# Performance work log

Hardware: AMD Instinct MI355X
Metric: run time of the kernel (lower is better)

Reference implementation:

```python
import jax, jax.numpy as jnp
import numpy as np

# dims: L layers, T steps, N envs, D d_model, H heads, DH d_head, M mem_len, DI d_inner
L, T, N, D, H, DH, M, DI = 6, 128, 32, 1024, 16, 64, 128, 4096


def _layer_norm(x, g, b, eps=1e-5):
    mu = jnp.mean(x, axis=-1, keepdims=True)
    var = jnp.mean(jnp.square(x - mu), axis=-1, keepdims=True)
    return (x - mu) * jax.lax.rsqrt(var + eps) * g + b


def _rel_shift(x):
    # x: (n, h, q, k) with k axis indexed by relative distance (k-1 .. 0)
    n, h, q, k = x.shape
    x = jnp.pad(x, ((0, 0), (0, 0), (0, 0), (1, 0)))
    x = x.reshape(n, h, k + 1, q)[:, :, 1:, :].reshape(n, h, q, k)
    return x


def setup_inputs() -> dict:
    key = jax.random.key(0)
    ks = jax.random.split(key, 16)
    s = 0.02
    inp = {
        "x": jax.random.normal(ks[0], (T * N, D), jnp.float32),
        "context": jax.random.normal(ks[1], (T * N, D), jnp.float32),
        "mems": jax.random.normal(ks[2], (L, N, M, D), jnp.float32),
        "masks": jnp.ones((T * N,), jnp.float32),
        "Wq": jax.random.normal(ks[3], (L, D, H * DH), jnp.float32) * s,
        "Wk": jax.random.normal(ks[4], (L, D, H * DH), jnp.float32) * s,
        "Wv": jax.random.normal(ks[5], (L, D, H * DH), jnp.float32) * s,
        "Wr": jax.random.normal(ks[6], (L, D, H * DH), jnp.float32) * s,
        "Wo": jax.random.normal(ks[7], (L, H * DH, D), jnp.float32) * s,
        "W1": jax.random.normal(ks[8], (L, D, DI), jnp.float32) * s,
        "b1": jnp.zeros((L, DI), jnp.float32),
        "W2": jax.random.normal(ks[9], (L, DI, D), jnp.float32) * s,
        "b2": jnp.zeros((L, D), jnp.float32),
        "ln1_g": jnp.ones((L, D), jnp.float32),
        "ln1_b": jnp.zeros((L, D), jnp.float32),
        "ln2_g": jnp.ones((L, D), jnp.float32),
        "ln2_b": jnp.zeros((L, D), jnp.float32),
        "r_w_bias": jax.random.normal(ks[10], (H, DH), jnp.float32) * s,
        "r_r_bias": jax.random.normal(ks[11], (H, DH), jnp.float32) * s,
    }
    return inp


def reference(x, context, mems, masks, Wq, Wk, Wv, Wr, Wo, W1, b1, W2, b2,
              ln1_g, ln1_b, ln2_g, ln2_b, r_w_bias, r_r_bias):
    n = mems.shape[1]
    t = x.shape[0] // n
    m = mems.shape[2]
    klen = m + t
    dh = r_w_bias.shape[-1]
    h_heads = r_w_bias.shape[0]

    xs = x.reshape(t, n, -1)
    ctx = context.reshape(t, n, -1)
    mk = masks.reshape(t, n)

    # zero memories for envs that reset at the first step (mems * masks)
    mems = mems * mk[0][None, :, None, None]

    # episode-reset attention mask: token i attends token j iff j<=i and no
    # reset (mask==0) happened between them; memory visible only before any reset
    ep = jnp.cumsum((mk == 0.0).astype(jnp.int32), axis=0)  # (t, n)
    epT = ep.T  # (n, t)
    causal = jnp.tril(jnp.ones((t, t), bool))
    allow_seq = causal[None, :, :] & (epT[:, :, None] == epT[:, None, :])  # (n,t,t)
    allow_mem = jnp.broadcast_to((epT == 0)[:, :, None], (n, t, m))  # (n,t,m)
    allow = jnp.concatenate([allow_mem, allow_seq], axis=-1)[:, None]  # (n,1,t,K)

    # sinusoidal relative position embedding, distances klen-1 .. 0
    pos = jnp.arange(klen - 1, -1, -1, dtype=x.dtype)
    inv_freq = 1.0 / (10000.0 ** (jnp.arange(0, xs.shape[-1], 2, dtype=x.dtype) / xs.shape[-1]))
    ang = pos[:, None] * inv_freq[None, :]
    R = jnp.concatenate([jnp.sin(ang), jnp.cos(ang)], axis=-1)  # (K, D)

    h = xs + ctx  # fuse observation features with goal context
    scale = 1.0 / jnp.sqrt(jnp.asarray(dh, x.dtype))

    n_layer = mems.shape[0]
    for l in range(n_layer):
        cat = jnp.concatenate([jnp.transpose(mems[l], (1, 0, 2)), h], axis=0)  # (K,n,D)
        q = (h @ Wq[l]).reshape(t, n, h_heads, dh)
        k = (cat @ Wk[l]).reshape(klen, n, h_heads, dh)
        v = (cat @ Wv[l]).reshape(klen, n, h_heads, dh)
        r = (R @ Wr[l]).reshape(klen, h_heads, dh)
        AC = jnp.einsum('inhd,jnhd->nhij', q + r_w_bias, k)
        BD = _rel_shift(jnp.einsum('inhd,jhd->nhij', q + r_r_bias, r))
        score = (AC + BD) * scale
        score = jnp.where(allow, score, -1e9)
        attn = jax.nn.softmax(score, axis=-1)
        o = jnp.einsum('nhij,jnhd->inhd', attn, v).reshape(t, n, h_heads * dh) @ Wo[l]
        h = _layer_norm(h + o, ln1_g[l], ln1_b[l])
        f = jax.nn.relu(h @ W1[l] + b1[l]) @ W2[l] + b2[l]
        h = _layer_norm(h + f, ln2_g[l], ln2_b[l])

    return h.reshape(t * n, -1)
```

## Files before the change

### kernel.cpp

```cpp
#include <hip/hip_runtime.h>
#include <stdint.h>

#define DEV static __device__ __forceinline__

typedef __attribute__((ext_vector_type(4))) float f32x4;
typedef __attribute__((ext_vector_type(8))) short bf16x8;
typedef __attribute__((ext_vector_type(4))) short s16x4;

static constexpr int L_ = 6, T_ = 128, NE = 32, D_ = 1024, H_ = 16, DH_ = 64, M_ = 128, DI_ = 4096;
static constexpr int KLEN = M_ + T_;
static constexpr int TN = T_ * NE;
static constexpr int NB = NE * H_;

DEV unsigned short f2bf(float f) {
  unsigned u = __builtin_bit_cast(unsigned, f);
  u += 0x7FFFu + ((u >> 16) & 1u);
  return (unsigned short)(u >> 16);
}
DEV float bf2f(unsigned short h) {
  unsigned u = ((unsigned)h) << 16;
  return __builtin_bit_cast(float, u);
}

DEV void gload16(const unsigned short* g, unsigned short* lds) {
  __builtin_amdgcn_global_load_lds(
      (const __attribute__((address_space(1))) unsigned int*)g,
      (__attribute__((address_space(3))) unsigned int*)lds, 16, 0, 0);
}

DEV void gemm_core(const unsigned short* __restrict__ Ab, int lda,
                   const unsigned short* __restrict__ Bb, int ldb,
                   unsigned short* lA, unsigned short* lB,
                   int m0, int n0, int nK, int w, int l,
                   f32x4 acc[4][4])
{
  const int wr = (w >> 1) * 64, wc = (w & 1) * 64;
  const int lan = l & 15, lgr = l >> 4;

  for (int kt = 0; kt < nK; ++kt) {
    const int k0 = kt * 64;
    __syncthreads();
#pragma unroll
    for (int i = 0; i < 4; ++i) {
      const int obb = i * 4096 + w * 1024;
      const int ob  = obb + (l << 4);
      const int row = ob >> 7;
      const int col = (((ob >> 4) & 7) ^ (row & 7)) << 3;
      gload16(Ab + (size_t)(m0 + row) * lda + k0 + col, lA + (obb >> 1));
      gload16(Bb + (size_t)(n0 + row) * ldb + k0 + col, lB + (obb >> 1));
    }
    asm volatile("s_waitcnt vmcnt(0)" ::: "memory");
    __syncthreads();

#pragma unroll
    for (int ks = 0; ks < 2; ++ks) {
      bf16x8 av[4], bv[4];
#pragma unroll
      for (int m = 0; m < 4; ++m) {
        const int row = wr + m * 16 + lan;
        const int byte = ((row << 7) + (ks << 6) + (lgr << 4)) ^ ((row & 7) << 4);
        av[m] = *(const bf16x8*)((const char*)lA + byte);
      }
#pragma unroll
      for (int n = 0; n < 4; ++n) {
        const int row = wc + n * 16 + lan;
        const int byte = ((row << 7) + (ks << 6) + (lgr << 4)) ^ ((row & 7) << 4);
        bv[n] = *(const bf16x8*)((const char*)lB + byte);
      }
#pragma unroll
      for (int m = 0; m < 4; ++m)
#pragma unroll
        for (int n = 0; n < 4; ++n)
          acc[m][n] = __builtin_amdgcn_mfma_f32_16x16x32_bf16(av[m], bv[n], acc[m][n], 0, 0, 0);
    }
  }
}

template <int EPI>
__global__ __launch_bounds__(256) void gemm_bt(
    const unsigned short* __restrict__ A, int lda, int sAn, int sAh,
    const unsigned short* __restrict__ B, int ldb, int sBn, int sBh,
    void* __restrict__ Cv, int ldc, int sC,
    const float* __restrict__ bias, int nK, int Hb)
{
  __shared__ unsigned short lA[128 * 64];
  __shared__ unsigned short lB[128 * 64];

  const int z = blockIdx.z;
  const int bn = z / Hb, bh = z % Hb;
  const unsigned short* Ab = A + (size_t)bn * sAn + (size_t)bh * sAh;
  const unsigned short* Bb = B + (size_t)bn * sBn + (size_t)bh * sBh;
  const int m0 = blockIdx.y * 128;
  const int n0 = blockIdx.x * 128;

  const int t = threadIdx.x;
  const int w = t >> 6, l = t & 63;
  const int wr = (w >> 1) * 64, wc = (w & 1) * 64;
  const int lan = l & 15, lgr = l >> 4;

  f32x4 acc[4][4];
#pragma unroll
  for (int m = 0; m < 4; ++m)
#pragma unroll
    for (int n = 0; n < 4; ++n) acc[m][n] = (f32x4){0.f, 0.f, 0.f, 0.f};

  gemm_core(Ab, lda, Bb, ldb, lA, lB, m0, n0, nK, w, l, acc);

  const int zc = z * sC;
#pragma unroll
  for (int m = 0; m < 4; ++m) {
    const int row = m0 + wr + m * 16 + lgr * 4;
#pragma unroll
    for (int n = 0; n < 4; ++n) {
      const int col = n0 + wc + n * 16 + lan;
      const float bcol = (EPI >= 2) ? bias[col] : 0.f;
#pragma unroll
      for (int e = 0; e < 4; ++e) {
        float v = acc[m][n][e];
        const size_t idx = (size_t)zc + (size_t)(row + e) * ldc + col;
        if (EPI == 0) {
          ((float*)Cv)[idx] = v;
        } else if (EPI == 1) {
          ((unsigned short*)Cv)[idx] = f2bf(v);
        } else if (EPI == 2) {
          v += bcol; v = v > 0.f ? v : 0.f;
          ((unsigned short*)Cv)[idx] = f2bf(v);
        } else {
          ((float*)Cv)[idx] = v + bcol;
        }
      }
    }
  }
}

__global__ __launch_bounds__(256) void gemm_proj(
    const unsigned short* __restrict__ catA, const unsigned short* __restrict__ wt,
    unsigned short* __restrict__ kb, unsigned short* __restrict__ vb,
    unsigned short* __restrict__ qw, unsigned short* __restrict__ qr,
    unsigned short* __restrict__ rb,
    const float* __restrict__ rwb, const float* __restrict__ rrb)
{
  __shared__ unsigned short lA[128 * 64];
  __shared__ unsigned short lB[128 * 64];

  const int id = blockIdx.x;
  int by, bx;
  if (id < 1024)      { by = id >> 4;               bx = id & 15; }
  else if (id < 1280) { const int u = id - 1024; by = 32 + (u >> 3); bx = 16 + (u & 7); }
  else                { const int u = id - 1280; by = 64 + (u >> 3); bx = 24 + (u & 7); }
  const int m0 = by * 128, n0 = bx * 128;

  const int t = threadIdx.x;
  const int w = t >> 6, l = t & 63;
  const int wr = (w >> 1) * 64, wc = (w & 1) * 64;
  const int lan = l & 15, lgr = l >> 4;

  f32x4 acc[4][4];
#pragma unroll
  for (int m = 0; m < 4; ++m)
#pragma unroll
    for (int n = 0; n < 4; ++n) acc[m][n] = (f32x4){0.f, 0.f, 0.f, 0.f};

  gemm_core(catA, 1024, wt, 1024, lA, lB, m0, n0, 16, w, l, acc);

#pragma unroll
  for (int m = 0; m < 4; ++m) {
    const int row = m0 + wr + m * 16 + lgr * 4;
#pragma unroll
    for (int n = 0; n < 4; ++n) {
      const int col = n0 + wc + n * 16 + lan;
#pragma unroll
      for (int e = 0; e < 4; ++e) {
        const float v = acc[m][n][e];
        const int r = row + e;
        if (col < 1024) {
          kb[(size_t)r * 1024 + col] = f2bf(v);
        } else if (col < 2048) {
          vb[(size_t)r * 1024 + col - 1024] = f2bf(v);
        } else if (col < 3072) {
          const int c = col - 2048;
          const size_t o = (size_t)(r - 4096) * 1024 + c;
          qw[o] = f2bf(v + rwb[c]);
          qr[o] = f2bf(v + rrb[c]);
        } else {
          const int c = col - 3072;
          rb[(size_t)(r - 8192) * 1024 + c] = f2bf(v);
        }
      }
    }
  }
}

__global__ __launch_bounds__(256) void pv_kernel(
    const unsigned short* __restrict__ P, const unsigned short* __restrict__ V,
    unsigned short* __restrict__ O)
{
  const int z = blockIdx.x;
  const int nn = z >> 4, hh = z & 15;
  const int t = threadIdx.x, w = t >> 6, l = t & 63;
  const int lan = l & 15, lgr = l >> 4;
  const int i0 = w * 32;
  const unsigned short* Pz = P + (size_t)z * (T_ * KLEN);
  const unsigned short* Vz = V + hh * DH_;

  f32x4 acc[2][4];
#pragma unroll
  for (int m = 0; m < 2; ++m)
#pragma unroll
    for (int n = 0; n < 4; ++n) acc[m][n] = (f32x4){0.f, 0.f, 0.f, 0.f};

  for (int ks = 0; ks < 8; ++ks) {
    const int kb = ks * 32 + lgr * 8;
    bf16x8 bv[4];
#pragma unroll
    for (int n = 0; n < 4; ++n) {
      const int d = n * 16 + lan;
      bf16x8 tmp;
#pragma unroll
      for (int jj = 0; jj < 8; ++jj)
        tmp[jj] = (short)Vz[(size_t)((kb + jj) * NE + nn) * 1024 + d];
      bv[n] = tmp;
    }
    bf16x8 av[2];
#pragma unroll
    for (int m = 0; m < 2; ++m)
      av[m] = *(const bf16x8*)&Pz[(size_t)(i0 + m * 16 + lan) * KLEN + kb];
#pragma unroll
    for (int m = 0; m < 2; ++m)
#pragma unroll
      for (int n = 0; n < 4; ++n)
        acc[m][n] = __builtin_amdgcn_mfma_f32_16x16x32_bf16(av[m], bv[n], acc[m][n], 0, 0, 0);
  }
#pragma unroll
  for (int m = 0; m < 2; ++m)
#pragma unroll
    for (int n = 0; n < 4; ++n)
#pragma unroll
      for (int e = 0; e < 4; ++e) {
        const int i = i0 + m * 16 + lgr * 4 + e;
        const int d = n * 16 + lan;
        O[(size_t)(i * NE + nn) * 1024 + hh * DH_ + d] = f2bf(acc[m][n][e]);
      }
}

__global__ __launch_bounds__(256) void softmax_kernel(
    const unsigned short* __restrict__ AC, const unsigned short* __restrict__ BD,
    const int* __restrict__ ep, unsigned short* __restrict__ P)
{
  const int g = blockIdx.x * 4 + (threadIdx.x >> 6);
  const int l = threadIdx.x & 63;
  const int z = g >> 7, i = g & 127;
  const int nn = z >> 4;
  const size_t base = (size_t)z * (T_ * KLEN) + (size_t)i * KLEN;
  const int j0 = l * 4;
  const int epi = ep[i * NE + nn];
  s16x4 ac4 = *(const s16x4*)&AC[base + j0];
  float sc[4];
#pragma unroll
  for (int q = 0; q < 4; ++q) {
    const int j = j0 + q;
    int jx = j + (T_ - 1) - i; if (jx > KLEN - 1) jx = KLEN - 1;
    const float bd = bf2f((unsigned short)BD[base + jx]);
    bool allow;
    if (j < M_) {
      allow = (epi == 0);
    } else {
      const int jp = j - M_;
      allow = (jp <= i) && (ep[jp * NE + nn] == epi);
    }
    const float v = (bf2f((unsigned short)ac4[q]) + bd) * 0.125f;
    sc[q] = allow ? v : -1e9f;
  }
  float mx = fmaxf(fmaxf(sc[0], sc[1]), fmaxf(sc[2], sc[3]));
#pragma unroll
  for (int o = 32; o; o >>= 1) mx = fmaxf(mx, __shfl_xor(mx, o));
  float p[4], sum = 0.f;
#pragma unroll
  for (int q = 0; q < 4; ++q) { p[q] = __expf(sc[q] - mx); sum += p[q]; }
#pragma unroll
  for (int o = 32; o; o >>= 1) sum += __shfl_xor(sum, o);
  const float inv = 1.f / sum;
  s16x4 o4;
#pragma unroll
  for (int q = 0; q < 4; ++q) o4[q] = (short)f2bf(p[q] * inv);
  *(s16x4*)&P[base + j0] = o4;
}

__global__ __launch_bounds__(256) void transpose_kernel(
    const float* __restrict__ W, unsigned short* __restrict__ WT, int Kd, int Nd)
{
  __shared__ float tile[32][33];
  const int tx = threadIdx.x & 31, ty = threadIdx.x >> 5;
  const int nIn = blockIdx.x * 32 + tx;
  const int kBase = blockIdx.y * 32;
#pragma unroll
  for (int r = 0; r < 32; r += 8)
    tile[ty + r][tx] = W[(size_t)(kBase + ty + r) * Nd + nIn];
  __syncthreads();
#pragma unroll
  for (int r = 0; r < 32; r += 8)
    WT[(size_t)(blockIdx.x * 32 + ty + r) * Kd + kBase + tx] = f2bf(tile[tx][ty + r]);
}

__global__ __launch_bounds__(256) void catmem_kernel(
    const float* __restrict__ mems_l, const float* __restrict__ masks,
    unsigned short* __restrict__ cat)
{
  const int idx = blockIdx.x * 256 + threadIdx.x;
  const int d = idx & 1023;
  const int r = idx >> 10;
  const int nn = r & 31, j = r >> 5;
  const float mk0 = masks[nn];
  cat[idx] = f2bf(mems_l[(size_t)(nn * M_ + j) * 1024 + d] * mk0);
}

__global__ __launch_bounds__(256) void hprep_kernel(
    const float* __restrict__ x, const float* __restrict__ ctx,
    float* __restrict__ h, unsigned short* __restrict__ catUp)
{
  const int idx = blockIdx.x * 256 + threadIdx.x;
  const float v = x[idx] + ctx[idx];
  h[idx] = v;
  catUp[idx] = f2bf(v);
}

__global__ __launch_bounds__(256) void rpos_kernel(unsigned short* __restrict__ R)
{
  const int idx = blockIdx.x * 256 + threadIdx.x;
  const int d = idx & 1023, j = idx >> 10;
  const float pos = (float)(KLEN - 1 - j);
  const int f = d & 511;
  const float inv_freq = __expf(-((float)(2 * f) * (1.f / 1024.f)) * 9.210340371976184f);
  const float ang = pos * inv_freq;
  const float v = (d < 512) ? sinf(ang) : cosf(ang);
  R[idx] = f2bf(v);
}

__global__ void ep_kernel(const float* __restrict__ masks, int* __restrict__ ep)
{
  const int nn = threadIdx.x;
  if (nn < NE) {
    int c = 0;
    for (int i = 0; i < T_; ++i) {
      c += (masks[i * NE + nn] == 0.f) ? 1 : 0;
      ep[i * NE + nn] = c;
    }
  }
}

__global__ __launch_bounds__(256) void ln_kernel(
    const float* __restrict__ a, const float* __restrict__ p0,
    const float* __restrict__ p1, const float* __restrict__ bias,
    const float* __restrict__ g, const float* __restrict__ bb,
    float* __restrict__ outf, unsigned short* __restrict__ outbf)
{
  const int row = blockIdx.x;
  const int t = threadIdx.x, w = t >> 6, l = t & 63;
  const int c = t * 4;
  const size_t base = (size_t)row * 1024;
  f32x4 va = *(const f32x4*)&a[base + c];
  f32x4 v0 = *(const f32x4*)&p0[base + c];
  f32x4 v1 = *(const f32x4*)&p1[base + c];
  f32x4 v = va + v0 + v1;
  if (bias) {
    f32x4 vb = *(const f32x4*)&bias[c];
    v = v + vb;
  }
  float s = v[0] + v[1] + v[2] + v[3];
#pragma unroll
  for (int o = 32; o; o >>= 1) s += __shfl_xor(s, o);
  __shared__ float red[8];
  if (l == 0) red[w] = s;
  __syncthreads();
  s = red[0] + red[1] + red[2] + red[3];
  const float mu = s * (1.f / 1024.f);
  f32x4 dv = v - mu;
  float s2 = dv[0]*dv[0] + dv[1]*dv[1] + dv[2]*dv[2] + dv[3]*dv[3];
#pragma unroll
  for (int o = 32; o; o >>= 1) s2 += __shfl_xor(s2, o);
  if (l == 0) red[4 + w] = s2;
  __syncthreads();
  s2 = red[4] + red[5] + red[6] + red[7];
  const float inv = rsqrtf(s2 * (1.f / 1024.f) + 1e-5f);
  f32x4 y;
#pragma unroll
  for (int q = 0; q < 4; ++q) y[q] = dv[q] * inv * g[c + q] + bb[c + q];
  *(f32x4*)&outf[base + c] = y;
  if (outbf) {
    s16x4 o4;
#pragma unroll
    for (int q = 0; q < 4; ++q) o4[q] = (short)f2bf(y[q]);
    *(s16x4*)&outbf[base + c] = o4;
  }
}

extern "C" void kernel_launch(void* const* d_in, const int* in_sizes, int n_in,
                              void* d_out, int out_size, void* d_ws, size_t ws_size,
                              hipStream_t stream)
{
  (void)in_sizes; (void)n_in; (void)out_size; (void)ws_size;
  const float* x    = (const float*)d_in[0];
  const float* ctx  = (const float*)d_in[1];
  const float* mems = (const float*)d_in[2];
  const float* masks= (const float*)d_in[3];
  const float* Wq   = (const float*)d_in[4];
  const float* Wk   = (const float*)d_in[5];
  const float* Wv   = (const float*)d_in[6];
  const float* Wr   = (const float*)d_in[7];
  const float* Wo   = (const float*)d_in[8];
  const float* W1   = (const float*)d_in[9];
  const float* b1   = (const float*)d_in[10];
  const float* W2   = (const float*)d_in[11];
  const float* b2   = (const float*)d_in[12];
  const float* ln1g = (const float*)d_in[13];
  const float* ln1b = (const float*)d_in[14];
  const float* ln2g = (const float*)d_in[15];
  const float* ln2b = (const float*)d_in[16];
  const float* rwb  = (const float*)d_in[17];
  const float* rrb  = (const float*)d_in[18];

  char* ws = (char*)d_ws;
  size_t off = 0;
  auto alloc = [&](size_t bytes) {
    char* p = ws + off;
    off += (bytes + 255) & ~(size_t)255;
    return p;
  };
  unsigned short* wtAll = (unsigned short*)alloc(4096u * 1024 * 2);
  unsigned short* wto = (unsigned short*)alloc(1024u * 1024 * 2);
  unsigned short* wt1 = (unsigned short*)alloc(4096u * 1024 * 2);
  unsigned short* wt2 = (unsigned short*)alloc(4096u * 1024 * 2);
  unsigned short* cat = (unsigned short*)alloc((size_t)(KLEN * NE + 256) * 1024 * 2);
  unsigned short* rbf = (unsigned short*)alloc((size_t)KLEN * 1024 * 2);
  int*            epb = (int*)alloc((size_t)T_ * NE * 4);
  float*          h   = (float*)alloc((size_t)TN * 1024 * 4);
  float*          h1  = (float*)alloc((size_t)TN * 1024 * 4);
  unsigned short* qw  = (unsigned short*)alloc((size_t)TN * 1024 * 2);
  unsigned short* qr  = (unsigned short*)alloc((size_t)TN * 1024 * 2);
  unsigned short* kbf = (unsigned short*)alloc((size_t)KLEN * NE * 1024 * 2);
  unsigned short* vbf = (unsigned short*)alloc((size_t)KLEN * NE * 1024 * 2);
  unsigned short* ACb = (unsigned short*)alloc((size_t)NB * T_ * KLEN * 2);
  unsigned short* BDb = (unsigned short*)alloc((size_t)NB * T_ * KLEN * 2);
  unsigned short* Pb  = (unsigned short*)alloc((size_t)NB * T_ * KLEN * 2);
  unsigned short* obf = (unsigned short*)alloc((size_t)TN * 1024 * 2);

  unsigned short* wtk = wtAll;
  unsigned short* wtv = wtAll + 1024u * 1024;
  unsigned short* wtq = wtAll + 2u * 1024 * 1024;
  unsigned short* wtr = wtAll + 3u * 1024 * 1024;
  unsigned short* catUp = cat + (size_t)M_ * NE * 1024;
  unsigned short* catR  = cat + (size_t)KLEN * NE * 1024;
  unsigned short* f1 = ACb;
  float* part = (float*)BDb;
  float* part1 = part + (size_t)TN * 1024;
  unsigned short* h1bf = qw;

  rpos_kernel<<<KLEN * 1024 / 256, 256, 0, stream>>>(catR);
  ep_kernel<<<1, 64, 0, stream>>>(masks, epb);
  hprep_kernel<<<TN * 1024 / 256, 256, 0, stream>>>(x, ctx, h, catUp);

  for (int l = 0; l < L_; ++l) {
    const size_t wOff = (size_t)l * 1024 * 1024;
    const size_t wOffBig = (size_t)l * 1024 * 4096;
    transpose_kernel<<<dim3(32, 32), 256, 0, stream>>>(Wk + wOff, wtk, 1024, 1024);
    transpose_kernel<<<dim3(32, 32), 256, 0, stream>>>(Wv + wOff, wtv, 1024, 1024);
    transpose_kernel<<<dim3(32, 32), 256, 0, stream>>>(Wq + wOff, wtq, 1024, 1024);
    transpose_kernel<<<dim3(32, 32), 256, 0, stream>>>(Wr + wOff, wtr, 1024, 1024);
    transpose_kernel<<<dim3(32, 32), 256, 0, stream>>>(Wo + wOff, wto, 1024, 1024);
    transpose_kernel<<<dim3(128, 32), 256, 0, stream>>>(W1 + wOffBig, wt1, 1024, 4096);
    transpose_kernel<<<dim3(32, 128), 256, 0, stream>>>(W2 + wOffBig, wt2, 4096, 1024);
    catmem_kernel<<<M_ * NE * 1024 / 256, 256, 0, stream>>>(
        mems + (size_t)l * NE * M_ * 1024, masks, cat);

    gemm_proj<<<1296, 256, 0, stream>>>(cat, wtAll, kbf, vbf, qw, qr, rbf, rwb, rrb);

    gemm_bt<1><<<dim3(2, 1, NB), 256, 0, stream>>>(qw, NE * 1024, 1024, 64,
                                                   kbf, NE * 1024, 1024, 64,
                                                   ACb, KLEN, T_ * KLEN, nullptr, 1, H_);
    gemm_bt<1><<<dim3(2, 1, NB), 256, 0, stream>>>(qr, NE * 1024, 1024, 64,
                                                   rbf, 1024, 0, 64,
                                                   BDb, KLEN, T_ * KLEN, nullptr, 1, H_);
    softmax_kernel<<<NB * T_ / 4, 256, 0, stream>>>(ACb, BDb, epb, Pb);
    pv_kernel<<<NB, 256, 0, stream>>>(Pb, vbf, obf);

    gemm_bt<0><<<dim3(8, 32, 2), 256, 0, stream>>>(obf, 1024, 0, 512,
                                                   wto, 1024, 0, 512,
                                                   part, 1024, TN * 1024, nullptr, 8, 2);
    ln_kernel<<<TN, 256, 0, stream>>>(h, part, part1, nullptr,
                                      ln1g + l * 1024, ln1b + l * 1024, h1, h1bf);

    gemm_bt<2><<<dim3(32, 32, 1), 256, 0, stream>>>(h1bf, 1024, 0, 0, wt1, 1024, 0, 0,
                                                    f1, 4096, 0, b1 + l * 4096, 16, 1);
    gemm_bt<0><<<dim3(8, 32, 2), 256, 0, stream>>>(f1, 4096, 0, 2048,
                                                   wt2, 4096, 0, 2048,
                                                   part, 1024, TN * 1024, nullptr, 32, 2);
    ln_kernel<<<TN, 256, 0, stream>>>(h1, part, part1, b2 + l * 1024,
                                      ln2g + l * 1024, ln2b + l * 1024,
                                      (l == L_ - 1) ? (float*)d_out : h, catUp);
  }
}
```

Before: 1.987 ms.

## Double-buffer LDS tiles in GEMM core and merge AC/BD score GEMMs

The shared GEMM core now uses two LDS buffers, issuing global-to-LDS loads for the next K tile before computing on the current one, which removes one barrier per iteration and overlaps memory latency with MFMA work. Shared memory per block doubles to 64KB, which may lower occupancy. The two per-layer score GEMM launches (AC and BD) are also merged into a single gemm_scores launch that picks its operands by block index, saving one launch and letting both run concurrently.

```diff
diff --git a/kernel.cpp b/kernel.cpp
--- a/kernel.cpp
+++ b/kernel.cpp
@@ -28,51 +28,66 @@
       (__attribute__((address_space(3))) unsigned int*)lds, 16, 0, 0);
 }
 
-DEV void gemm_core(const unsigned short* __restrict__ Ab, int lda,
-                   const unsigned short* __restrict__ Bb, int ldb,
-                   unsigned short* lA, unsigned short* lB,
-                   int m0, int n0, int nK, int w, int l,
-                   f32x4 acc[4][4])
+DEV void stage128(const unsigned short* __restrict__ Ab, int lda,
+                  const unsigned short* __restrict__ Bb, int ldb,
+                  unsigned short* lA, unsigned short* lB,
+                  int m0, int n0, int k0, int w, int l)
+{
+#pragma unroll
+  for (int i = 0; i < 4; ++i) {
+    const int obb = i * 4096 + w * 1024;
+    const int ob  = obb + (l << 4);
+    const int row = ob >> 7;
+    const int col = (((ob >> 4) & 7) ^ (row & 7)) << 3;
+    gload16(Ab + (size_t)(m0 + row) * lda + k0 + col, lA + (obb >> 1));
+    gload16(Bb + (size_t)(n0 + row) * ldb + k0 + col, lB + (obb >> 1));
+  }
+}
+
+DEV void compute128(const unsigned short* lA, const unsigned short* lB,
+                    int w, int l, f32x4 acc[4][4])
 {
   const int wr = (w >> 1) * 64, wc = (w & 1) * 64;
   const int lan = l & 15, lgr = l >> 4;
-
+#pragma unroll
+  for (int ks = 0; ks < 2; ++ks) {
+    bf16x8 av[4], bv[4];
+#pragma unroll
+    for (int m = 0; m < 4; ++m) {
+      const int row = wr + m * 16 + lan;
+      const int byte = ((row << 7) + (ks << 6) + (lgr << 4)) ^ ((row & 7) << 4);
+      av[m] = *(const bf16x8*)((const char*)lA + byte);
+    }
+#pragma unroll
+    for (int n = 0; n < 4; ++n) {
+      const int row = wc + n * 16 + lan;
+      const int byte = ((row << 7) + (ks << 6) + (lgr << 4)) ^ ((row & 7) << 4);
+      bv[n] = *(const bf16x8*)((const char*)lB + byte);
+    }
+#pragma unroll
+    for (int m = 0; m < 4; ++m)
+#pragma unroll
+      for (int n = 0; n < 4; ++n)
+        acc[m][n] = __builtin_amdgcn_mfma_f32_16x16x32_bf16(av[m], bv[n], acc[m][n], 0, 0, 0);
+  }
+}
+
+DEV void gemm128_2ph(const unsigned short* __restrict__ Ab, int lda,
+                     const unsigned short* __restrict__ Bb, int ldb,
+                     unsigned short (*shA)[8192], unsigned short (*shB)[8192],
+                     int m0, int n0, int nK, int w, int l, f32x4 acc[4][4])
+{
+  stage128(Ab, lda, Bb, ldb, shA[0], shB[0], m0, n0, 0, w, l);
+  asm volatile("s_waitcnt vmcnt(0)" ::: "memory");
+  __syncthreads();
+  int cur = 0;
   for (int kt = 0; kt < nK; ++kt) {
-    const int k0 = kt * 64;
-    __syncthreads();
-#pragma unroll
-    for (int i = 0; i < 4; ++i) {
-      const int obb = i * 4096 + w * 1024;
-      const int ob  = obb + (l << 4);
-      const int row = ob >> 7;
-      const int col = (((ob >> 4) & 7) ^ (row & 7)) << 3;
-      gload16(Ab + (size_t)(m0 + row) * lda + k0 + col, lA + (obb >> 1));
-      gload16(Bb + (size_t)(n0 + row) * ldb + k0 + col, lB + (obb >> 1));
-    }
+    if (kt + 1 < nK)
+      stage128(Ab, lda, Bb, ldb, shA[cur ^ 1], shB[cur ^ 1], m0, n0, (kt + 1) * 64, w, l);
+    compute128(shA[cur], shB[cur], w, l, acc);
     asm volatile("s_waitcnt vmcnt(0)" ::: "memory");
     __syncthreads();
-
-#pragma unroll
-    for (int ks = 0; ks < 2; ++ks) {
-      bf16x8 av[4], bv[4];
-#pragma unroll
-      for (int m = 0; m < 4; ++m) {
-        const int row = wr + m * 16 + lan;
-        const int byte = ((row << 7) + (ks << 6) + (lgr << 4)) ^ ((row & 7) << 4);
-        av[m] = *(const bf16x8*)((const char*)lA + byte);
-      }
-#pragma unroll
-      for (int n = 0; n < 4; ++n) {
-        const int row = wc + n * 16 + lan;
-        const int byte = ((row << 7) + (ks << 6) + (lgr << 4)) ^ ((row & 7) << 4);
-        bv[n] = *(const bf16x8*)((const char*)lB + byte);
-      }
-#pragma unroll
-      for (int m = 0; m < 4; ++m)
-#pragma unroll
-        for (int n = 0; n < 4; ++n)
-          acc[m][n] = __builtin_amdgcn_mfma_f32_16x16x32_bf16(av[m], bv[n], acc[m][n], 0, 0, 0);
-    }
+    cur ^= 1;
   }
 }
 
@@ -83,8 +98,8 @@
     void* __restrict__ Cv, int ldc, int sC,
     const float* __restrict__ bias, int nK, int Hb)
 {
-  __shared__ unsigned short lA[128 * 64];
-  __shared__ unsigned short lB[128 * 64];
+  __shared__ unsigned short shA[2][8192];
+  __shared__ unsigned short shB[2][8192];
 
   const int z = blockIdx.z;
   const int bn = z / Hb, bh = z % Hb;
@@ -104,7 +119,7 @@
 #pragma unroll
     for (int n = 0; n < 4; ++n) acc[m][n] = (f32x4){0.f, 0.f, 0.f, 0.f};
 
-  gemm_core(Ab, lda, Bb, ldb, lA, lB, m0, n0, nK, w, l, acc);
+  gemm128_2ph(Ab, lda, Bb, ldb, shA, shB, m0, n0, nK, w, l, acc);
 
   const int zc = z * sC;
 #pragma unroll
@@ -140,8 +155,8 @@
     unsigned short* __restrict__ rb,
     const float* __restrict__ rwb, const float* __restrict__ rrb)
 {
-  __shared__ unsigned short lA[128 * 64];
-  __shared__ unsigned short lB[128 * 64];
+  __shared__ unsigned short shA[2][8192];
+  __shared__ unsigned short shB[2][8192];
 
   const int id = blockIdx.x;
   int by, bx;
@@ -161,7 +176,7 @@
 #pragma unroll
     for (int n = 0; n < 4; ++n) acc[m][n] = (f32x4){0.f, 0.f, 0.f, 0.f};
 
-  gemm_core(catA, 1024, wt, 1024, lA, lB, m0, n0, 16, w, l, acc);
+  gemm128_2ph(catA, 1024, wt, 1024, shA, shB, m0, n0, 16, w, l, acc);
 
 #pragma unroll
   for (int m = 0; m < 4; ++m) {
@@ -187,6 +202,51 @@
           rb[(size_t)(r - 8192) * 1024 + c] = f2bf(v);
         }
       }
+    }
+  }
+}
+
+__global__ __launch_bounds__(256) void gemm_scores(
+    const unsigned short* __restrict__ qw, const unsigned short* __restrict__ qr,
+    const unsigned short* __restrict__ kbf, const unsigned short* __restrict__ rbf,
+    unsigned short* __restrict__ AC, unsigned short* __restrict__ BD)
+{
+  __shared__ unsigned short shA[2][8192];
+  __shared__ unsigned short shB[2][8192];
+
+  const int bx = blockIdx.x;
+  const int z = blockIdx.y;
+  const int nn = z >> 4, hh = z & 15;
+  const bool isBD = bx >= 2;
+  const int n0 = (bx & 1) * 128;
+  const unsigned short* Ab = (isBD ? qr : qw) + (size_t)nn * 1024 + hh * 64;
+  const unsigned short* Bb = isBD ? (rbf + hh * 64)
+                                  : (kbf + (size_t)nn * 1024 + hh * 64);
+  const int ldb = isBD ? 1024 : (NE * 1024);
+  unsigned short* C = (isBD ? BD : AC) + (size_t)z * (T_ * KLEN);
+
+  const int t = threadIdx.x;
+  const int w = t >> 6, l = t & 63;
+  const int wr = (w >> 1) * 64, wc = (w & 1) * 64;
+  const int lan = l & 15, lgr = l >> 4;
+
+  f32x4 acc[4][4];
+#pragma unroll
+  for (int m = 0; m < 4; ++m)
+#pragma unroll
+    for (int n = 0; n < 4; ++n) acc[m][n] = (f32x4){0.f, 0.f, 0.f, 0.f};
+
+  gemm128_2ph(Ab, NE * 1024, Bb, ldb, shA, shB, 0, n0, 1, w, l, acc);
+
+#pragma unroll
+  for (int m = 0; m < 4; ++m) {
+    const int row = wr + m * 16 + lgr * 4;
+#pragma unroll
+    for (int n = 0; n < 4; ++n) {
+      const int col = n0 + wc + n * 16 + lan;
+#pragma unroll
+      for (int e = 0; e < 4; ++e)
+        C[(size_t)(row + e) * KLEN + col] = f2bf(acc[m][n][e]);
     }
   }
 }
@@ -474,12 +534,8 @@
 
     gemm_proj<<<1296, 256, 0, stream>>>(cat, wtAll, kbf, vbf, qw, qr, rbf, rwb, rrb);
 
-    gemm_bt<1><<<dim3(2, 1, NB), 256, 0, stream>>>(qw, NE * 1024, 1024, 64,
-                                                   kbf, NE * 1024, 1024, 64,
-                                                   ACb, KLEN, T_ * KLEN, nullptr, 1, H_);
-    gemm_bt<1><<<dim3(2, 1, NB), 256, 0, stream>>>(qr, NE * 1024, 1024, 64,
-                                                   rbf, 1024, 0, 64,
-                                                   BDb, KLEN, T_ * KLEN, nullptr, 1, H_);
+    gemm_scores<<<dim3(4, 512), 256, 0, stream>>>(qw, qr, kbf, rbf, ACb, BDb);
+
     softmax_kernel<<<NB * T_ / 4, 256, 0, stream>>>(ACb, BDb, epb, Pb);
     pv_kernel<<<NB, 256, 0, stream>>>(Pb, vbf, obf);
 
```

New measurement: 1.939 ms. 2.4% less time.
